# Kernel optimization log

Hardware: AMD Instinct MI355X
Metric: run time of the kernel (lower is better)

## Reference

```python
import jax, jax.numpy as jnp
import numpy as np

NUM_HEADS = 16
HIDDEN = 1024
HEAD_DIM = HIDDEN // NUM_HEADS


def setup_inputs() -> dict:
    key = jax.random.key(0)
    ks = jax.random.split(key, 8)
    B, S = 4, 1024
    scale = 0.02
    return {
        "hidden_states": jax.random.normal(ks[0], (B, S, HIDDEN), jnp.float32),
        "attention_mask": jnp.zeros((B, 1, 1, S), jnp.float32),
        "Wq": jax.random.normal(ks[1], (HIDDEN, HIDDEN), jnp.float32) * scale,
        "bq": jnp.zeros((HIDDEN,), jnp.float32),
        "Wk": jax.random.normal(ks[2], (HIDDEN, HIDDEN), jnp.float32) * scale,
        "bk": jnp.zeros((HIDDEN,), jnp.float32),
        "Wv": jax.random.normal(ks[3], (HIDDEN, HIDDEN), jnp.float32) * scale,
        "bv": jnp.zeros((HIDDEN,), jnp.float32),
    }


def _split_heads(x):
    # [B,S,H] -> [B,heads,S,head_dim]
    B, S, _ = x.shape
    return x.reshape(B, S, NUM_HEADS, HEAD_DIM).transpose(0, 2, 1, 3)


def reference(hidden_states, attention_mask, Wq, bq, Wk, bk, Wv, bv):
    # torch.nn.Linear convention: y = x @ W.T + b
    q = _split_heads(hidden_states @ Wq.T + bq)
    k = _split_heads(hidden_states @ Wk.T + bk)
    v = _split_heads(hidden_states @ Wv.T + bv)
    scores = jnp.einsum('bhqd,bhkd->bhqk', q, k) * (HEAD_DIM ** -0.5)
    scores = scores + attention_mask  # broadcast [B,1,1,S]
    probs = jax.nn.softmax(scores, axis=-1)
    context = jnp.einsum('bhqk,bhkd->bhqd', probs, v)  # [B,heads,S,head_dim]
    B, _, S, _ = context.shape
    return context.transpose(0, 2, 1, 3).reshape(B, S, HIDDEN)
```

## Files before the change

kernel.cpp:

```cpp
#include <hip/hip_runtime.h>
#include <hip/hip_bf16.h>
#include <stdint.h>

#define NH 16
#define HID 1024
#define HD 64
#define NB 4
#define SS 1024
#define MTOT (NB*SS)

typedef __attribute__((ext_vector_type(8))) short bf16x8;
typedef __attribute__((ext_vector_type(4))) float f32x4;
typedef __attribute__((ext_vector_type(16))) float f32x16;

#define LOG2E 1.44269504088896f

__device__ __forceinline__ unsigned short f2bf(float f) {
  union { float f; unsigned u; } v; v.f = f;
  unsigned u = v.u;
  return (unsigned short)((u + 0x7FFFu + ((u >> 16) & 1u)) >> 16);
}

__device__ __forceinline__ unsigned cvtpk(float lo, float hi) {
  unsigned r;
  asm("v_cvt_pk_bf16_f32 %0, %1, %2" : "=v"(r) : "v"(lo), "v"(hi));
  return r;
}

__device__ __forceinline__ void pl32swap(unsigned &a, unsigned &b) {
  asm("v_permlane32_swap_b32 %0, %1" : "+v"(a), "+v"(b));
}

__device__ __forceinline__ float exp2fast(float x) {
  float r;
  asm("v_exp_f32 %0, %1" : "=v"(r) : "v"(x));
  return r;
}

__device__ __forceinline__ void async16(void* lds, const void* g) {
  __builtin_amdgcn_global_load_lds(
      (const __attribute__((address_space(1))) unsigned*)g,
      (__attribute__((address_space(3))) unsigned*)lds, 16, 0, 0);
}

__global__ void cvt_all(const float4* __restrict__ X,
                        const float4* __restrict__ Wq,
                        const float4* __restrict__ Wk,
                        const float4* __restrict__ Wv,
                        ushort4* __restrict__ Xb,
                        ushort4* __restrict__ Wb) {
  int i = blockIdx.x * 256 + threadIdx.x;
  const float4* src; ushort4* dst; int idx;
  if (i < (MTOT * HID / 4)) {
    src = X; dst = Xb; idx = i;
  } else {
    int j = i - (MTOT * HID / 4);
    int sel = j >> 18;
    idx = j & 262143;
    src = (sel == 0) ? Wq : (sel == 1) ? Wk : Wv;
    dst = Wb + (size_t)sel * 262144;
  }
  float4 v = src[idx];
  ushort4 o;
  o.x = f2bf(v.x); o.y = f2bf(v.y); o.z = f2bf(v.z); o.w = f2bf(v.w);
  dst[idx] = o;
}

__global__ __launch_bounds__(256) void qkv_gemm(
    const ushort* __restrict__ Xb,
    const ushort* __restrict__ Wb,
    const float* __restrict__ bq,
    const float* __restrict__ bk,
    const float* __restrict__ bv,
    ushort* __restrict__ Q,
    ushort* __restrict__ K,
    ushort* __restrict__ Vt)
{
  __shared__ ushort Al[128 * 64];
  __shared__ ushort Bl[128 * 64];

  int bid = blockIdx.x;
  int swz = (bid & 7) * 96 + (bid >> 3);
  const int nbn = 3072 / 128;
  int bm = swz / nbn, bn = swz % nbn;
  int m0 = bm * 128, n0 = bn * 128;

  int tid = threadIdx.x;
  int wave = tid >> 6, lane = tid & 63;
  int g = lane >> 4, c = lane & 15;
  int wr = wave >> 1, wc = wave & 1;

  const ushort* Asrc = Xb + (size_t)(m0 + (tid >> 3)) * 1024 + (tid & 7) * 8;
  const ushort* Bsrc = Wb + (size_t)(n0 + (tid >> 3)) * 1024 + (tid & 7) * 8;

  f32x4 acc[4][4] = {};

  for (int ks = 0; ks < 16; ++ks) {
    int k0 = ks * 64;
    __syncthreads();
    #pragma unroll
    for (int i = 0; i < 4; ++i) {
      async16((char*)Al + i * 4096 + wave * 1024, Asrc + (size_t)i * 32 * 1024 + k0);
      async16((char*)Bl + i * 4096 + wave * 1024, Bsrc + (size_t)i * 32 * 1024 + k0);
    }
    __syncthreads();
    #pragma unroll
    for (int kk = 0; kk < 2; ++kk) {
      bf16x8 a[4], b[4];
      #pragma unroll
      for (int m = 0; m < 4; ++m)
        a[m] = *(const bf16x8*)((const char*)Al + (wr * 64 + m * 16 + c) * 128 + kk * 64 + g * 16);
      #pragma unroll
      for (int n = 0; n < 4; ++n)
        b[n] = *(const bf16x8*)((const char*)Bl + (wc * 64 + n * 16 + c) * 128 + kk * 64 + g * 16);
      #pragma unroll
      for (int m = 0; m < 4; ++m)
        #pragma unroll
        for (int n = 0; n < 4; ++n)
          acc[m][n] = __builtin_amdgcn_mfma_f32_16x16x32_bf16(a[m], b[n], acc[m][n], 0, 0, 0);
    }
  }

  int sel = n0 >> 10;
  const float* bp = (sel == 0) ? bq : (sel == 1) ? bk : bv;
  float scl = (sel == 0) ? 0.125f * LOG2E : 1.0f;

  #pragma unroll
  for (int n = 0; n < 4; ++n) {
    int nn = (n0 & 1023) + wc * 64 + n * 16 + c;
    float bias = bp[nn];
    int h = nn >> 6, d = nn & 63;
    #pragma unroll
    for (int m = 0; m < 4; ++m) {
      int rowg = m0 + wr * 64 + m * 16 + g * 4;
      int bb = rowg >> 10;
      int s = rowg & 1023;
      #pragma unroll
      for (int r = 0; r < 4; ++r) {
        float val = (acc[m][n][r] + bias) * scl;
        unsigned short ob = f2bf(val);
        if (sel == 0)
          Q[(size_t)((bb * 16 + h) * 1024 + s + r) * 64 + d] = ob;
        else if (sel == 1)
          K[(size_t)((bb * 16 + h) * 1024 + s + r) * 64 + d] = ob;
        else
          Vt[(size_t)((bb * 16 + h) * 64 + d) * 1024 + s + r] = ob;
      }
    }
  }
}

__device__ __forceinline__ void build_pa(const f32x16& p, bf16x8& pa0, bf16x8& pa1) {
  unsigned W0 = cvtpk(p[0],  p[1]);
  unsigned W1 = cvtpk(p[2],  p[3]);
  unsigned W2 = cvtpk(p[4],  p[5]);
  unsigned W3 = cvtpk(p[6],  p[7]);
  unsigned W4 = cvtpk(p[8],  p[9]);
  unsigned W5 = cvtpk(p[10], p[11]);
  unsigned W6 = cvtpk(p[12], p[13]);
  unsigned W7 = cvtpk(p[14], p[15]);
  pl32swap(W0, W2);
  pl32swap(W1, W3);
  pl32swap(W4, W6);
  pl32swap(W5, W7);
  union { unsigned u[4]; bf16x8 v; } a0, a1;
  a0.u[0] = W0; a0.u[1] = W1; a0.u[2] = W2; a0.u[3] = W3;
  a1.u[0] = W4; a1.u[1] = W5; a1.u[2] = W6; a1.u[3] = W7;
  pa0 = a0.v; pa1 = a1.v;
}

__global__ __launch_bounds__(256) void attn(
    const ushort* __restrict__ Q,
    const ushort* __restrict__ K,
    const ushort* __restrict__ Vt,
    const float* __restrict__ mask,
    float* __restrict__ out)
{
  __shared__ __attribute__((aligned(16))) char kv_lds[2][16384];

  int blk = blockIdx.x;
  int xcd = blk & 7;
  int j = blk >> 3;
  int bh = xcd * 8 + (j >> 3);
  int qt = j & 7;
  int b = bh >> 4, h = bh & 15;
  int tid = threadIdx.x, wave = tid >> 6, lane = tid & 63;
  int r31 = lane & 31, hi = lane >> 5;
  int rsw = r31 & 7;
  int hib = hi << 4;
  int q0 = qt * 128 + wave * 32;

  const ushort* Qb = Q + (size_t)bh * SS * 64;
  const ushort* Kb = K + (size_t)bh * SS * 64;
  const ushort* Vb = Vt + (size_t)bh * 64 * SS;
  const float* mb = mask + b * SS;

  bf16x8 qf[4];
  #pragma unroll
  for (int kp = 0; kp < 4; ++kp)
    qf[kp] = *(const bf16x8*)(Qb + (size_t)(q0 + r31) * 64 + kp * 16 + hi * 8);

  int srow = lane >> 3;
  int schunk = lane & 7;
  const ushort* sptr[4];
  int soff[4];
  #pragma unroll
  for (int j2 = 0; j2 < 4; ++j2) {
    soff[j2] = wave * 4096 + j2 * 1024;
    if (wave < 2) {
      int row = wave * 32 + j2 * 8 + srow;
      sptr[j2] = Kb + (size_t)row * 64 + ((schunk ^ srow) << 3);
    } else {
      int d = (wave - 2) * 32 + j2 * 8 + srow;
      sptr[j2] = Vb + (size_t)d * SS + ((schunk ^ srow) << 3);
    }
  }
  const int sstep = (wave < 2) ? 64 * 64 : 64;

#define STAGE(bufidx) do {                              \
    char* lb_ = kv_lds[bufidx];                         \
    async16(lb_ + soff[0], sptr[0]);                    \
    async16(lb_ + soff[1], sptr[1]);                    \
    async16(lb_ + soff[2], sptr[2]);                    \
    async16(lb_ + soff[3], sptr[3]);                    \
    sptr[0] += sstep; sptr[1] += sstep;                 \
    sptr[2] += sstep; sptr[3] += sstep;                 \
  } while (0)

  f32x16 o0 = (f32x16)0.0f, o1 = (f32x16)0.0f;
  float mrow = 0.f, lrow = 0.f;

  STAGE(0);

  for (int it = 0; it < 16; ++it) {
    int cur = it & 1;
    if (it < 15) {
      STAGE(cur ^ 1);
      asm volatile("s_waitcnt vmcnt(4)" ::: "memory");
    } else {
      asm volatile("s_waitcnt vmcnt(0)" ::: "memory");
    }
    __builtin_amdgcn_sched_barrier(0);
    __builtin_amdgcn_s_barrier();
    __builtin_amdgcn_sched_barrier(0);

    const char* kb0 = kv_lds[cur];
    const char* vb0 = kv_lds[cur] + 8192;

    f32x16 s0 = (f32x16)0.0f, s1 = (f32x16)0.0f;
    __builtin_amdgcn_s_setprio(1);
    #pragma unroll
    for (int kp = 0; kp < 4; ++kp) {
      int ch = (((kp << 1) | hi) ^ rsw) << 4;
      bf16x8 ka = *(const bf16x8*)(kb0 + r31 * 128 + ch);
      bf16x8 kc = *(const bf16x8*)(kb0 + (32 + r31) * 128 + ch);
      s0 = __builtin_amdgcn_mfma_f32_32x32x16_bf16(ka, qf[kp], s0, 0, 0, 0);
      s1 = __builtin_amdgcn_mfma_f32_32x32x16_bf16(kc, qf[kp], s1, 0, 0, 0);
    }
    __builtin_amdgcn_s_setprio(0);

    int kv = it * 64;
    #pragma unroll
    for (int sq = 0; sq < 4; ++sq) {
      f32x4 mk0 = *(const f32x4*)(mb + kv + sq * 8 + hi * 4);
      f32x4 mk1 = *(const f32x4*)(mb + kv + 32 + sq * 8 + hi * 4);
      #pragma unroll
      for (int r = 0; r < 4; ++r) {
        s0[sq * 4 + r] = fmaf(mk0[r], LOG2E, s0[sq * 4 + r]);
        s1[sq * 4 + r] = fmaf(mk1[r], LOG2E, s1[sq * 4 + r]);
      }
    }

    float mx = s0[0];
    #pragma unroll
    for (int i = 1; i < 16; ++i) mx = fmaxf(mx, s0[i]);
    #pragma unroll
    for (int i = 0; i < 16; ++i) mx = fmaxf(mx, s1[i]);
    mx = fmaxf(mx, __shfl_xor(mx, 32));

    if (!__all(mx <= mrow + 11.5416f)) {
      float mn = fmaxf(mrow, mx);
      float sc = exp2fast(mrow - mn);
      mrow = mn;
      lrow *= sc;
      #pragma unroll
      for (int i = 0; i < 16; ++i) {
        int qh = (i & 3) + 8 * (i >> 2);
        float scq = __uint_as_float((unsigned)__builtin_amdgcn_ds_bpermute(
            (qh << 2) + hib, (int)__float_as_uint(sc)));
        o0[i] *= scq; o1[i] *= scq;
      }
    }

    f32x16 p0, p1;
    float rs = 0.f;
    #pragma unroll
    for (int i = 0; i < 16; ++i) { float e = exp2fast(s0[i] - mrow); p0[i] = e; rs += e; }
    #pragma unroll
    for (int i = 0; i < 16; ++i) { float e = exp2fast(s1[i] - mrow); p1[i] = e; rs += e; }
    rs += __shfl_xor(rs, 32);
    lrow += rs;

    #pragma unroll
    for (int T = 0; T < 2; ++T) {
      bf16x8 pa0, pa1;
      build_pa(T ? p1 : p0, pa0, pa1);
      __builtin_amdgcn_s_setprio(1);
      #pragma unroll
      for (int kh = 0; kh < 2; ++kh) {
        int kap = 2 * T + kh;
        int ch = (((kap << 1) | hi) ^ rsw) << 4;
        bf16x8 va = *(const bf16x8*)(vb0 + r31 * 128 + ch);
        bf16x8 vc = *(const bf16x8*)(vb0 + (32 + r31) * 128 + ch);
        bf16x8 pf = kh ? pa1 : pa0;
        o0 = __builtin_amdgcn_mfma_f32_32x32x16_bf16(pf, va, o0, 0, 0, 0);
        o1 = __builtin_amdgcn_mfma_f32_32x32x16_bf16(pf, vc, o1, 0, 0, 0);
      }
      __builtin_amdgcn_s_setprio(0);
    }

    __builtin_amdgcn_sched_barrier(0);
    __builtin_amdgcn_s_barrier();
  }
#undef STAGE

  float inv = 1.0f / lrow;
  #pragma unroll
  for (int i = 0; i < 16; ++i) {
    int qh = (i & 3) + 8 * (i >> 2);
    float li = __uint_as_float((unsigned)__builtin_amdgcn_ds_bpermute(
        (qh << 2) + hib, (int)__float_as_uint(inv)));
    int row = q0 + qh + 4 * hi;
    float* op = out + (size_t)(b * SS + row) * 1024 + h * 64 + r31;
    op[0]  = o0[i] * li;
    op[32] = o1[i] * li;
  }
}

extern "C" void kernel_launch(void* const* d_in, const int* in_sizes, int n_in,
                              void* d_out, int out_size, void* d_ws, size_t ws_size,
                              hipStream_t stream) {
  const float* hs   = (const float*)d_in[0];
  const float* mask = (const float*)d_in[1];
  const float* Wq   = (const float*)d_in[2];
  const float* bq   = (const float*)d_in[3];
  const float* Wk   = (const float*)d_in[4];
  const float* bk   = (const float*)d_in[5];
  const float* Wv   = (const float*)d_in[6];
  const float* bv   = (const float*)d_in[7];
  float* out = (float*)d_out;

  char* ws = (char*)d_ws;
  ushort* Xb = (ushort*)(ws);
  ushort* Wb = (ushort*)(ws + (8u  << 20));
  ushort* Qp = (ushort*)(ws + (14u << 20));
  ushort* Kp = (ushort*)(ws + (22u << 20));
  ushort* Vt = (ushort*)(ws + (30u << 20));

  cvt_all<<<7168, 256, 0, stream>>>((const float4*)hs, (const float4*)Wq,
                                    (const float4*)Wk, (const float4*)Wv,
                                    (ushort4*)Xb, (ushort4*)Wb);
  qkv_gemm<<<768, 256, 0, stream>>>(Xb, Wb, bq, bk, bv, Qp, Kp, Vt);
  attn<<<512, 256, 0, stream>>>(Qp, Kp, Vt, mask, out);
}
```

Baseline: 87.99 us.

## Double-buffer QKV GEMM LDS tiles with XOR swizzle and async prefetch

The QKV projection GEMM now splits K into 32-wide stages and double-buffers the LDS A/B tiles, so the global-to-LDS async loads for the next stage are issued before computing on the current one. A partial vmcnt wait lets those loads stay in flight. An XOR swizzle on the 16-byte chunk index is meant to cut LDS bank conflicts on the MFMA operand reads, and setprio raises wave priority around the MFMA block. In exchange there are twice as many barriers per K, and each stage has a shorter MFMA run between them.

```diff
diff --git a/kernel.cpp b/kernel.cpp
--- a/kernel.cpp
+++ b/kernel.cpp
@@ -76,8 +76,8 @@
     ushort* __restrict__ K,
     ushort* __restrict__ Vt)
 {
-  __shared__ ushort Al[128 * 64];
-  __shared__ ushort Bl[128 * 64];
+  __shared__ __attribute__((aligned(16))) ushort Al[2][128 * 32];
+  __shared__ __attribute__((aligned(16))) ushort Bl[2][128 * 32];
 
   int bid = blockIdx.x;
   int swz = (bid & 7) * 96 + (bid >> 3);
@@ -90,36 +90,63 @@
   int g = lane >> 4, c = lane & 15;
   int wr = wave >> 1, wc = wave & 1;
 
-  const ushort* Asrc = Xb + (size_t)(m0 + (tid >> 3)) * 1024 + (tid & 7) * 8;
-  const ushort* Bsrc = Wb + (size_t)(n0 + (tid >> 3)) * 1024 + (tid & 7) * 8;
+  int srow = tid >> 2;
+  int schunk = tid & 3;
+  int ssw = (srow >> 1) & 3;
+  const ushort* Asrc0 = Xb + (size_t)(m0 + srow) * 1024 + ((schunk ^ ssw) << 3);
+  const ushort* Asrc1 = Xb + (size_t)(m0 + 64 + srow) * 1024 + ((schunk ^ ssw) << 3);
+  const ushort* Bsrc0 = Wb + (size_t)(n0 + srow) * 1024 + ((schunk ^ ssw) << 3);
+  const ushort* Bsrc1 = Wb + (size_t)(n0 + 64 + srow) * 1024 + ((schunk ^ ssw) << 3);
+  int soff = srow * 64 + schunk * 16;
+
+#define GSTAGE(bi) do {                                   \
+    char* la_ = (char*)Al[bi]; char* lb_ = (char*)Bl[bi]; \
+    async16(la_ + soff,        Asrc0);                    \
+    async16(la_ + 4096 + soff, Asrc1);                    \
+    async16(lb_ + soff,        Bsrc0);                    \
+    async16(lb_ + 4096 + soff, Bsrc1);                    \
+    Asrc0 += 32; Asrc1 += 32; Bsrc0 += 32; Bsrc1 += 32;   \
+  } while (0)
 
   f32x4 acc[4][4] = {};
-
-  for (int ks = 0; ks < 16; ++ks) {
-    int k0 = ks * 64;
-    __syncthreads();
-    #pragma unroll
-    for (int i = 0; i < 4; ++i) {
-      async16((char*)Al + i * 4096 + wave * 1024, Asrc + (size_t)i * 32 * 1024 + k0);
-      async16((char*)Bl + i * 4096 + wave * 1024, Bsrc + (size_t)i * 32 * 1024 + k0);
-    }
-    __syncthreads();
-    #pragma unroll
-    for (int kk = 0; kk < 2; ++kk) {
-      bf16x8 a[4], b[4];
-      #pragma unroll
-      for (int m = 0; m < 4; ++m)
-        a[m] = *(const bf16x8*)((const char*)Al + (wr * 64 + m * 16 + c) * 128 + kk * 64 + g * 16);
+  int rsw = (c >> 1) & 3;
+  int ch = ((g ^ rsw) << 4);
+
+  GSTAGE(0);
+
+  for (int ks = 0; ks < 32; ++ks) {
+    int cur = ks & 1;
+    if (ks < 31) {
+      GSTAGE(cur ^ 1);
+      asm volatile("s_waitcnt vmcnt(4)" ::: "memory");
+    } else {
+      asm volatile("s_waitcnt vmcnt(0)" ::: "memory");
+    }
+    __builtin_amdgcn_sched_barrier(0);
+    __builtin_amdgcn_s_barrier();
+    __builtin_amdgcn_sched_barrier(0);
+
+    const char* la = (const char*)Al[cur];
+    const char* lb = (const char*)Bl[cur];
+    bf16x8 a[4], b[4];
+    #pragma unroll
+    for (int m = 0; m < 4; ++m)
+      a[m] = *(const bf16x8*)(la + (wr * 64 + m * 16 + c) * 64 + ch);
+    #pragma unroll
+    for (int n = 0; n < 4; ++n)
+      b[n] = *(const bf16x8*)(lb + (wc * 64 + n * 16 + c) * 64 + ch);
+    __builtin_amdgcn_s_setprio(1);
+    #pragma unroll
+    for (int m = 0; m < 4; ++m)
       #pragma unroll
       for (int n = 0; n < 4; ++n)
-        b[n] = *(const bf16x8*)((const char*)Bl + (wc * 64 + n * 16 + c) * 128 + kk * 64 + g * 16);
-      #pragma unroll
-      for (int m = 0; m < 4; ++m)
-        #pragma unroll
-        for (int n = 0; n < 4; ++n)
-          acc[m][n] = __builtin_amdgcn_mfma_f32_16x16x32_bf16(a[m], b[n], acc[m][n], 0, 0, 0);
-    }
-  }
+        acc[m][n] = __builtin_amdgcn_mfma_f32_16x16x32_bf16(a[m], b[n], acc[m][n], 0, 0, 0);
+    __builtin_amdgcn_s_setprio(0);
+
+    __builtin_amdgcn_sched_barrier(0);
+    __builtin_amdgcn_s_barrier();
+  }
+#undef GSTAGE
 
   int sel = n0 >> 10;
   const float* bp = (sel == 0) ? bq : (sel == 1) ? bk : bv;
```

Result: no change. 87.15 us (-0.9%).
